# Kernel optimization log

Measured on AMD Instinct MI355X. Metric: run time of the kernel, lower is better.

## Reference

```python
import jax, jax.numpy as jnp
import numpy as np

NUM_LAYERS = 2
NUM_RES_LAYERS = 1  # residual add applied to layers i >= NUM_LAYERS - NUM_RES_LAYERS


def _lstm_seq(x, W, U, b, reverse):
    """Keras-style LSTM over full sequence. x:[B,T,E], W:[E,4H], U:[H,4H], b:[4H].
    Gate order i,f,g,o (Keras). reverse=True emulates go_backwards + K.reverse
    (lax.scan reverse=True keeps outputs time-aligned). Returns [B,T,H]."""
    B = x.shape[0]
    H = U.shape[0]
    # precompute input projections for all timesteps in one big matmul
    zx = jnp.einsum('bte,eg->btg', x, W) + b  # [B,T,4H]
    zx = jnp.swapaxes(zx, 0, 1)  # [T,B,4H]

    def step(carry, zxt):
        h, c = carry
        z = zxt + h @ U  # [B,4H]
        i, f, g, o = jnp.split(z, 4, axis=-1)
        i = jax.nn.sigmoid(i)
        f = jax.nn.sigmoid(f)
        g = jnp.tanh(g)
        o = jax.nn.sigmoid(o)
        c = f * c + i * g
        h = o * jnp.tanh(c)
        return (h, c), h

    init = (jnp.zeros((B, H), x.dtype), jnp.zeros((B, H), x.dtype))
    _, hs = jax.lax.scan(step, init, zx, reverse=reverse)  # [T,B,H]
    return jnp.swapaxes(hs, 0, 1)


def setup_inputs() -> dict:
    key = jax.random.key(0)
    k1, k2, k3 = jax.random.split(key, 3)
    B, T, E, H = 512, 200, 128, 128
    s = 0.05  # keep gates in a sane regime
    x = jax.random.normal(k1, (B, T, E), dtype=jnp.float32)
    W = jax.random.normal(k2, (NUM_LAYERS, 2, E, 4 * H), dtype=jnp.float32) * s
    U = jax.random.normal(k3, (NUM_LAYERS, 2, H, 4 * H), dtype=jnp.float32) * s
    b = jnp.ones((NUM_LAYERS, 2, 4 * H), dtype=jnp.float32)  # bias_initializer='ones'
    return {"x": x, "W": W, "U": U, "b": b}


def reference(x, W, U, b):
    # inference mode: dropout inactive
    input_fw = x
    input_bw = x
    for i in range(NUM_LAYERS):
        out_fw = _lstm_seq(input_fw, W[i, 0], U[i, 0], b[i, 0], reverse=False)
        out_bw = _lstm_seq(input_bw, W[i, 1], U[i, 1], b[i, 1], reverse=True)
        if i >= NUM_LAYERS - NUM_RES_LAYERS:
            out_fw = out_fw + input_fw
            out_bw = out_bw + input_bw
        input_fw = out_fw
        input_bw = out_bw
    # mode == 'ave'
    return (input_fw + input_bw) / 2
```

## Files before the change

kernel.cpp:

```cpp
#include <hip/hip_runtime.h>


typedef _Float16 f16;
typedef _Float16 f16x4 __attribute__((ext_vector_type(4)));
typedef _Float16 f16x8 __attribute__((ext_vector_type(8)));
typedef float    f32x4 __attribute__((ext_vector_type(4)));

#define B_   512
#define T_   200
#define E_   128
#define H_   128
#define G4_  512
#define M_   (B_*T_)

static __device__ __forceinline__ float rcpf_(float x) {
#if __has_builtin(__builtin_amdgcn_rcpf)
  return __builtin_amdgcn_rcpf(x);
#else
  return 1.f / x;
#endif
}
static __device__ __forceinline__ float sigm(float x) { return rcpf_(1.f + __expf(-x)); }
static __device__ __forceinline__ float tanh_(float x) { return 2.f * rcpf_(1.f + __expf(-2.f * x)) - 1.f; }

static __device__ __forceinline__ void lgkm_barrier() {
  asm volatile("s_waitcnt lgkmcnt(0)" ::: "memory");
  __builtin_amdgcn_s_barrier();
}

template <typename AT> struct InPipe;
template <> struct InPipe<float> {
  float4 r[8];
  __device__ __forceinline__ void load(const float* p, int kg) {
#pragma unroll
    for (int kk = 0; kk < 4; ++kk) {
      r[kk * 2]     = *(const float4*)(p + kk * 32 + kg * 8);
      r[kk * 2 + 1] = *(const float4*)(p + kk * 32 + kg * 8 + 4);
    }
  }
  __device__ __forceinline__ void get(f16x8 xf[4]) const {
#pragma unroll
    for (int kk = 0; kk < 4; ++kk) {
      f16x8 v;
      v[0] = (f16)r[kk*2].x;     v[1] = (f16)r[kk*2].y;
      v[2] = (f16)r[kk*2].z;     v[3] = (f16)r[kk*2].w;
      v[4] = (f16)r[kk*2+1].x;   v[5] = (f16)r[kk*2+1].y;
      v[6] = (f16)r[kk*2+1].z;   v[7] = (f16)r[kk*2+1].w;
      xf[kk] = v;
    }
  }
};
template <> struct InPipe<f16> {
  f16x8 r[4];
  __device__ __forceinline__ void load(const f16* p, int kg) {
#pragma unroll
    for (int kk = 0; kk < 4; ++kk) r[kk] = *(const f16x8*)(p + kk * 32 + kg * 8);
  }
  __device__ __forceinline__ void get(f16x8 xf[4]) const {
#pragma unroll
    for (int kk = 0; kk < 4; ++kk) xf[kk] = r[kk];
  }
};

template <int LAYER, typename AT>
__global__ __launch_bounds__(512, 2)
void scan_fused(const AT* __restrict__ in,
                const float* __restrict__ Ul,
                const float* __restrict__ Wl,
                const float* __restrict__ bl,
                const f16* __restrict__ res,
                f16* __restrict__ hout)
{
  __shared__ f16 hsh[2][16][136];

  const int tid  = threadIdx.x;
  const int lane = tid & 63;
  const int wv   = tid >> 6;
  const int row  = lane & 15;
  const int kg   = lane >> 4;
  const int bx   = blockIdx.x;
  const int dir  = bx >> 5;
  const int R0   = (bx & 31) * 16;
  const int coff = wv * 16 + kg * 4;

  const float* Ud = Ul + (size_t)dir * H_ * G4_;
  const float* Wd = Wl + (size_t)dir * E_ * G4_;
  const float* bd = bl + (size_t)dir * G4_;
  const AT* ind   = in + (LAYER == 1 ? (size_t)dir * M_ * H_ : 0);
  f16* houtd      = hout + (size_t)dir * M_ * H_;

  f16x8 aU[4][4], aW[4][4];
#pragma unroll
  for (int g = 0; g < 4; ++g) {
    const int gcol = g * 128 + wv * 16 + row;
#pragma unroll
    for (int kk = 0; kk < 4; ++kk) {
      f16x8 vu, vw;
#pragma unroll
      for (int j = 0; j < 8; ++j) {
        const size_t k = (size_t)(kk * 32 + kg * 8 + j);
        vu[j] = (f16)Ud[k * G4_ + gcol];
        vw[j] = (f16)Wd[k * G4_ + gcol];
      }
      aU[g][kk] = vu;
      aW[g][kk] = vw;
    }
  }
  f32x4 zb[4];
#pragma unroll
  for (int g = 0; g < 4; ++g) {
#pragma unroll
    for (int i = 0; i < 4; ++i) zb[g][i] = bd[g * 128 + coff + i];
  }

  for (int i = tid; i < 2 * 16 * 136; i += 512) ((f16*)hsh)[i] = (f16)0.f;

  const int t0 = dir ? (T_ - 1) : 0;
  const int ts = dir ? -1 : 1;

  const AT*  inrow  = ind + (size_t)(R0 + row) * T_ * E_;
  const f16* resrow = (LAYER == 1) ? res + (size_t)dir * M_ * H_ + (size_t)(R0 + row) * T_ * H_
                                   : nullptr;
  f16* outrow = houtd + (size_t)(R0 + row) * T_ * H_;

  float cc[4] = {0.f, 0.f, 0.f, 0.f};

  InPipe<AT> xpA, xpB;
  f16x4 rvA = {}, rvB = {};
  xpA.load(inrow + (size_t)t0 * E_, kg);
  xpB.load(inrow + (size_t)(t0 + ts) * E_, kg);
  if (LAYER == 1) {
    rvA = *(const f16x4*)(resrow + (size_t)t0 * H_ + coff);
    rvB = *(const f16x4*)(resrow + (size_t)(t0 + ts) * H_ + coff);
  }

  lgkm_barrier();

  auto step = [&](InPipe<AT>& xp, f16x4& rv, int s, int rp, int wp) {
    const int t = t0 + s * ts;

    f16x8 xf[4];
    xp.get(xf);
    float rvf[4];
    if (LAYER == 1) {
#pragma unroll
      for (int i = 0; i < 4; ++i) rvf[i] = (float)rv[i];
    }
    {
      const int spf = s + 2;
      const size_t tpf = (spf < T_) ? (size_t)(t0 + spf * ts) : (size_t)t0;
      xp.load(inrow + tpf * E_, kg);
      if (LAYER == 1) rv = *(const f16x4*)(resrow + tpf * H_ + coff);
    }

    f32x4 z0 = zb[0], z1 = zb[1], z2 = zb[2], z3 = zb[3];
#pragma unroll
    for (int kk = 0; kk < 4; ++kk) {
      z0 = __builtin_amdgcn_mfma_f32_16x16x32_f16(aW[0][kk], xf[kk], z0, 0, 0, 0);
      z1 = __builtin_amdgcn_mfma_f32_16x16x32_f16(aW[1][kk], xf[kk], z1, 0, 0, 0);
      z2 = __builtin_amdgcn_mfma_f32_16x16x32_f16(aW[2][kk], xf[kk], z2, 0, 0, 0);
      z3 = __builtin_amdgcn_mfma_f32_16x16x32_f16(aW[3][kk], xf[kk], z3, 0, 0, 0);
    }
    f16x8 hf[4];
#pragma unroll
    for (int kk = 0; kk < 4; ++kk) hf[kk] = *(const f16x8*)&hsh[rp][row][kk * 32 + kg * 8];
#pragma unroll
    for (int kk = 0; kk < 4; ++kk) {
      z0 = __builtin_amdgcn_mfma_f32_16x16x32_f16(aU[0][kk], hf[kk], z0, 0, 0, 0);
      z1 = __builtin_amdgcn_mfma_f32_16x16x32_f16(aU[1][kk], hf[kk], z1, 0, 0, 0);
      z2 = __builtin_amdgcn_mfma_f32_16x16x32_f16(aU[2][kk], hf[kk], z2, 0, 0, 0);
      z3 = __builtin_amdgcn_mfma_f32_16x16x32_f16(aU[3][kk], hf[kk], z3, 0, 0, 0);
    }

    float hv[4];
#pragma unroll
    for (int i = 0; i < 4; ++i) {
      const float ig = sigm(z0[i]);
      const float fg = sigm(z1[i]);
      const float gg = tanh_(z2[i]);
      const float og = sigm(z3[i]);
      cc[i] = fg * cc[i] + ig * gg;
      hv[i] = og * tanh_(cc[i]);
    }
    f16x4 hp;
#pragma unroll
    for (int i = 0; i < 4; ++i) hp[i] = (f16)hv[i];
    *(f16x4*)&hsh[wp][row][coff] = hp;

    f16* orow = outrow + (size_t)t * H_ + coff;
    if (LAYER == 0) {
      *(f16x4*)orow = hp;
    } else {
      f16x4 o;
#pragma unroll
      for (int i = 0; i < 4; ++i) o[i] = (f16)(0.5f * (hv[i] + rvf[i]));
      *(f16x4*)orow = o;
    }

    lgkm_barrier();
  };

  for (int k = 0; k < T_ / 2; ++k) {
    step(xpA, rvA, 2 * k,     0, 1);
    step(xpB, rvB, 2 * k + 1, 1, 0);
  }
}

__global__ __launch_bounds__(256)
void final_add(const f16* __restrict__ a, const f16* __restrict__ b,
               float* __restrict__ o)
{
  const int n8 = M_ * H_ / 8;
  for (int i = blockIdx.x * 256 + threadIdx.x; i < n8; i += gridDim.x * 256) {
    const f16x8 va = *(const f16x8*)(a + (size_t)i * 8);
    const f16x8 vb = *(const f16x8*)(b + (size_t)i * 8);
    float4 o0, o1;
    o0.x = (float)va[0] + (float)vb[0];  o0.y = (float)va[1] + (float)vb[1];
    o0.z = (float)va[2] + (float)vb[2];  o0.w = (float)va[3] + (float)vb[3];
    o1.x = (float)va[4] + (float)vb[4];  o1.y = (float)va[5] + (float)vb[5];
    o1.z = (float)va[6] + (float)vb[6];  o1.w = (float)va[7] + (float)vb[7];
    *(float4*)(o + (size_t)i * 8)     = o0;
    *(float4*)(o + (size_t)i * 8 + 4) = o1;
  }
}

extern "C" void kernel_launch(void* const* d_in, const int* in_sizes, int n_in,
                              void* d_out, int out_size, void* d_ws, size_t ws_size,
                              hipStream_t stream) {
  const float* x = (const float*)d_in[0];
  const float* W = (const float*)d_in[1];
  const float* U = (const float*)d_in[2];
  const float* b = (const float*)d_in[3];
  float* out = (float*)d_out;

  f16* h0 = (f16*)d_ws;
  f16* h1 = h0 + (size_t)2 * M_ * H_;

  const size_t WL = (size_t)2 * E_ * G4_;
  const size_t BL = 2 * G4_;

  scan_fused<0, float><<<dim3(64), 512, 0, stream>>>(x, U, W, b, nullptr, h0);
  scan_fused<1, f16><<<dim3(64), 512, 0, stream>>>(h0, U + WL, W + WL, b + BL, h0, h1);
  final_add<<<dim3(2048), 256, 0, stream>>>(h1, h1 + (size_t)M_ * H_, out);
}
```

Measured before the change: 726.6 us.

## Pre-convert x to fp16 and transpose weights to fp16 in prep kernels

Adds a conversion kernel that turns the fp32 input x into fp16 before the layer-0 scan, so that scan streams half the bytes per step and skips in-loop conversion. Adds a kernel that transposes W and U into fp16 gate-major layout, so the scan loads its weight fragments with vector loads instead of scalar strided fp32 loads. Also moves the LDS load of h ahead of the input-projection MFMAs to hide latency. The cost is two extra launches and an extra full pass over x, which is memory traffic outside the latency-bound scan.

```diff
diff --git a/kernel.cpp b/kernel.cpp
--- a/kernel.cpp
+++ b/kernel.cpp
@@ -28,45 +28,36 @@
   __builtin_amdgcn_s_barrier();
 }
 
-template <typename AT> struct InPipe;
-template <> struct InPipe<float> {
-  float4 r[8];
-  __device__ __forceinline__ void load(const float* p, int kg) {
-#pragma unroll
-    for (int kk = 0; kk < 4; ++kk) {
-      r[kk * 2]     = *(const float4*)(p + kk * 32 + kg * 8);
-      r[kk * 2 + 1] = *(const float4*)(p + kk * 32 + kg * 8 + 4);
-    }
-  }
-  __device__ __forceinline__ void get(f16x8 xf[4]) const {
-#pragma unroll
-    for (int kk = 0; kk < 4; ++kk) {
-      f16x8 v;
-      v[0] = (f16)r[kk*2].x;     v[1] = (f16)r[kk*2].y;
-      v[2] = (f16)r[kk*2].z;     v[3] = (f16)r[kk*2].w;
-      v[4] = (f16)r[kk*2+1].x;   v[5] = (f16)r[kk*2+1].y;
-      v[6] = (f16)r[kk*2+1].z;   v[7] = (f16)r[kk*2+1].w;
-      xf[kk] = v;
-    }
-  }
-};
-template <> struct InPipe<f16> {
-  f16x8 r[4];
-  __device__ __forceinline__ void load(const f16* p, int kg) {
-#pragma unroll
-    for (int kk = 0; kk < 4; ++kk) r[kk] = *(const f16x8*)(p + kk * 32 + kg * 8);
-  }
-  __device__ __forceinline__ void get(f16x8 xf[4]) const {
-#pragma unroll
-    for (int kk = 0; kk < 4; ++kk) xf[kk] = r[kk];
-  }
-};
-
-template <int LAYER, typename AT>
+__global__ __launch_bounds__(256)
+void cvt_x(const float* __restrict__ x, f16* __restrict__ xh) {
+  const int n8 = M_ * E_ / 8;
+  for (int i = blockIdx.x * 256 + threadIdx.x; i < n8; i += gridDim.x * 256) {
+    const float4 a = ((const float4*)x)[i * 2];
+    const float4 b = ((const float4*)x)[i * 2 + 1];
+    f16x8 v;
+    v[0] = (f16)a.x; v[1] = (f16)a.y; v[2] = (f16)a.z; v[3] = (f16)a.w;
+    v[4] = (f16)b.x; v[5] = (f16)b.y; v[6] = (f16)b.z; v[7] = (f16)b.w;
+    *(f16x8*)(xh + (size_t)i * 8) = v;
+  }
+}
+
+__global__ __launch_bounds__(256)
+void prep_w(const float* __restrict__ W, const float* __restrict__ U,
+            f16* __restrict__ Wt, f16* __restrict__ Ut) {
+  const int m = blockIdx.x;
+  const float* s = (m < 4 ? W + (size_t)m * E_ * G4_ : U + (size_t)(m - 4) * E_ * G4_);
+  f16* d        = (m < 4 ? Wt + (size_t)m * E_ * G4_ : Ut + (size_t)(m - 4) * E_ * G4_);
+  for (int i = threadIdx.x; i < E_ * G4_; i += 256) {
+    const int k = i >> 9, g = i & 511;
+    d[(size_t)g * E_ + k] = (f16)s[i];
+  }
+}
+
+template <int LAYER>
 __global__ __launch_bounds__(512, 2)
-void scan_fused(const AT* __restrict__ in,
-                const float* __restrict__ Ul,
-                const float* __restrict__ Wl,
+void scan_fused(const f16* __restrict__ in,
+                const f16* __restrict__ Utl,
+                const f16* __restrict__ Wtl,
                 const float* __restrict__ bl,
                 const f16* __restrict__ res,
                 f16* __restrict__ hout)
@@ -83,27 +74,20 @@
   const int R0   = (bx & 31) * 16;
   const int coff = wv * 16 + kg * 4;
 
-  const float* Ud = Ul + (size_t)dir * H_ * G4_;
-  const float* Wd = Wl + (size_t)dir * E_ * G4_;
+  const f16* Ud = Utl + (size_t)dir * G4_ * E_;
+  const f16* Wd = Wtl + (size_t)dir * G4_ * E_;
   const float* bd = bl + (size_t)dir * G4_;
-  const AT* ind   = in + (LAYER == 1 ? (size_t)dir * M_ * H_ : 0);
+  const f16* ind  = in + (LAYER == 1 ? (size_t)dir * M_ * H_ : 0);
   f16* houtd      = hout + (size_t)dir * M_ * H_;
 
   f16x8 aU[4][4], aW[4][4];
 #pragma unroll
   for (int g = 0; g < 4; ++g) {
-    const int gcol = g * 128 + wv * 16 + row;
-#pragma unroll
-    for (int kk = 0; kk < 4; ++kk) {
-      f16x8 vu, vw;
-#pragma unroll
-      for (int j = 0; j < 8; ++j) {
-        const size_t k = (size_t)(kk * 32 + kg * 8 + j);
-        vu[j] = (f16)Ud[k * G4_ + gcol];
-        vw[j] = (f16)Wd[k * G4_ + gcol];
-      }
-      aU[g][kk] = vu;
-      aW[g][kk] = vw;
+    const size_t gcol = (size_t)(g * 128 + wv * 16 + row) * E_;
+#pragma unroll
+    for (int kk = 0; kk < 4; ++kk) {
+      aU[g][kk] = *(const f16x8*)(Ud + gcol + kk * 32 + kg * 8);
+      aW[g][kk] = *(const f16x8*)(Wd + gcol + kk * 32 + kg * 8);
     }
   }
   f32x4 zb[4];
@@ -118,38 +102,53 @@
   const int t0 = dir ? (T_ - 1) : 0;
   const int ts = dir ? -1 : 1;
 
-  const AT*  inrow  = ind + (size_t)(R0 + row) * T_ * E_;
-  const f16* resrow = (LAYER == 1) ? res + (size_t)dir * M_ * H_ + (size_t)(R0 + row) * T_ * H_
-                                   : nullptr;
+  const f16* inrow  = ind + (size_t)(R0 + row) * T_ * E_;
+  const f16* resrow = (LAYER == 1)
+      ? res + (size_t)dir * M_ * H_ + (size_t)(R0 + row) * T_ * H_ : nullptr;
   f16* outrow = houtd + (size_t)(R0 + row) * T_ * H_;
 
   float cc[4] = {0.f, 0.f, 0.f, 0.f};
 
-  InPipe<AT> xpA, xpB;
+  f16x8 xA[4], xB[4];
   f16x4 rvA = {}, rvB = {};
-  xpA.load(inrow + (size_t)t0 * E_, kg);
-  xpB.load(inrow + (size_t)(t0 + ts) * E_, kg);
-  if (LAYER == 1) {
-    rvA = *(const f16x4*)(resrow + (size_t)t0 * H_ + coff);
-    rvB = *(const f16x4*)(resrow + (size_t)(t0 + ts) * H_ + coff);
+  {
+    const f16* pA = inrow + (size_t)t0 * E_;
+    const f16* pB = inrow + (size_t)(t0 + ts) * E_;
+#pragma unroll
+    for (int kk = 0; kk < 4; ++kk) {
+      xA[kk] = *(const f16x8*)(pA + kk * 32 + kg * 8);
+      xB[kk] = *(const f16x8*)(pB + kk * 32 + kg * 8);
+    }
+    if (LAYER == 1) {
+      rvA = *(const f16x4*)(resrow + (size_t)t0 * H_ + coff);
+      rvB = *(const f16x4*)(resrow + (size_t)(t0 + ts) * H_ + coff);
+    }
   }
 
   lgkm_barrier();
 
-  auto step = [&](InPipe<AT>& xp, f16x4& rv, int s, int rp, int wp) {
+  auto step = [&](f16x8 (&xp)[4], f16x4& rv, int s, int rp, int wp) {
     const int t = t0 + s * ts;
 
+    f16x8 hf[4];
+#pragma unroll
+    for (int kk = 0; kk < 4; ++kk) hf[kk] = *(const f16x8*)&hsh[rp][row][kk * 32 + kg * 8];
+
     f16x8 xf[4];
-    xp.get(xf);
+#pragma unroll
+    for (int kk = 0; kk < 4; ++kk) xf[kk] = xp[kk];
     float rvf[4];
     if (LAYER == 1) {
 #pragma unroll
       for (int i = 0; i < 4; ++i) rvf[i] = (float)rv[i];
     }
+
     {
       const int spf = s + 2;
       const size_t tpf = (spf < T_) ? (size_t)(t0 + spf * ts) : (size_t)t0;
-      xp.load(inrow + tpf * E_, kg);
+      const f16* p = inrow + tpf * E_;
+#pragma unroll
+      for (int kk = 0; kk < 4; ++kk) xp[kk] = *(const f16x8*)(p + kk * 32 + kg * 8);
       if (LAYER == 1) rv = *(const f16x4*)(resrow + tpf * H_ + coff);
     }
 
@@ -161,9 +160,6 @@
       z2 = __builtin_amdgcn_mfma_f32_16x16x32_f16(aW[2][kk], xf[kk], z2, 0, 0, 0);
       z3 = __builtin_amdgcn_mfma_f32_16x16x32_f16(aW[3][kk], xf[kk], z3, 0, 0, 0);
     }
-    f16x8 hf[4];
-#pragma unroll
-    for (int kk = 0; kk < 4; ++kk) hf[kk] = *(const f16x8*)&hsh[rp][row][kk * 32 + kg * 8];
 #pragma unroll
     for (int kk = 0; kk < 4; ++kk) {
       z0 = __builtin_amdgcn_mfma_f32_16x16x32_f16(aU[0][kk], hf[kk], z0, 0, 0, 0);
@@ -201,8 +197,8 @@
   };
 
   for (int k = 0; k < T_ / 2; ++k) {
-    step(xpA, rvA, 2 * k,     0, 1);
-    step(xpB, rvB, 2 * k + 1, 1, 0);
+    step(xA, rvA, 2 * k,     0, 1);
+    step(xB, rvB, 2 * k + 1, 1, 0);
   }
 }
 
@@ -233,13 +229,19 @@
   const float* b = (const float*)d_in[3];
   float* out = (float*)d_out;
 
-  f16* h0 = (f16*)d_ws;
+  char* ws = (char*)d_ws;
+  f16* xh = (f16*)ws;
+  f16* h0 = xh + (size_t)M_ * E_;
   f16* h1 = h0 + (size_t)2 * M_ * H_;
-
-  const size_t WL = (size_t)2 * E_ * G4_;
-  const size_t BL = 2 * G4_;
-
-  scan_fused<0, float><<<dim3(64), 512, 0, stream>>>(x, U, W, b, nullptr, h0);
-  scan_fused<1, f16><<<dim3(64), 512, 0, stream>>>(h0, U + WL, W + WL, b + BL, h0, h1);
+  f16* Wt = h1 + (size_t)2 * M_ * H_;
+  f16* Ut = Wt + (size_t)4 * G4_ * E_;
+
+  const size_t WTL = (size_t)2 * G4_ * E_;
+  const size_t BL  = 2 * G4_;
+
+  cvt_x<<<dim3(2048), 256, 0, stream>>>(x, xh);
+  prep_w<<<dim3(8), 256, 0, stream>>>(W, U, Wt, Ut);
+  scan_fused<0><<<dim3(64), 512, 0, stream>>>(xh, Ut, Wt, b, nullptr, h0);
+  scan_fused<1><<<dim3(64), 512, 0, stream>>>(h0, Ut + WTL, Wt + WTL, b + BL, h0, h1);
   final_add<<<dim3(2048), 256, 0, stream>>>(h1, h1 + (size_t)M_ * H_, out);
 }
```

Result: faster. 684.8 us (-5.8%).
